# Performance work log

Hardware: AMD Instinct MI355X
Metric: run time of the kernel (lower is better)

The kernel has to match this reference:

```python
import jax, jax.numpy as jnp
import numpy as np

B, C, H, W = 2, 128, 32, 48
D_INNER = 2 * C          # expand=2
D_STATE = 16
DT_RANK = int(np.ceil(C / 16))
K = 4                    # four scan directions
EPS = 1e-5


def setup_inputs() -> dict:
    ks = jax.random.split(jax.random.key(0), 8)
    return {
        "rgb": jax.random.normal(ks[0], (B, C, H, W), jnp.float32),
        "t": jax.random.normal(ks[1], (B, C, H, W), jnp.float32),
        "in_proj_w": jax.random.normal(ks[2], (2 * D_INNER, C), jnp.float32) / np.float32(np.sqrt(C)),
        "conv_w": jax.random.normal(ks[3], (D_INNER, 1, 3, 3), jnp.float32) / 3.0,
        "conv_b": jnp.zeros((D_INNER,), jnp.float32),
        "x_proj_w": jax.random.normal(ks[4], (K, DT_RANK + 2 * D_STATE, D_INNER), jnp.float32) / np.float32(np.sqrt(D_INNER)),
        "dt_projs_w": jax.random.normal(ks[5], (K, D_INNER, DT_RANK), jnp.float32) * np.float32(DT_RANK ** -0.5),
        "dt_projs_b": jax.random.uniform(ks[6], (K, D_INNER), jnp.float32, minval=1e-4, maxval=0.1),
        "A_logs": jnp.log(jnp.tile(jnp.arange(1, D_STATE + 1, dtype=jnp.float32), (K * D_INNER, 1))),
        "Ds": jnp.ones((K * D_INNER,), jnp.float32),
        "out_norm_g": jnp.ones((D_INNER,), jnp.float32),
        "out_norm_b": jnp.zeros((D_INNER,), jnp.float32),
        "out_proj_w": jax.random.normal(ks[7], (C, D_INNER), jnp.float32) / np.float32(np.sqrt(D_INNER)),
    }


def _selective_scan(u, delta, A, Bmat, Cmat, Dvec):
    """u, delta: (B,K,D,L); A: (K,D,N); Bmat/Cmat: (B,K,N,L); Dvec: (K,D)."""
    uT = jnp.moveaxis(u, -1, 0)      # (L,B,K,D)
    dT = jnp.moveaxis(delta, -1, 0)  # (L,B,K,D)
    BT = jnp.moveaxis(Bmat, -1, 0)   # (L,B,K,N)
    CT = jnp.moveaxis(Cmat, -1, 0)   # (L,B,K,N)
    h0 = jnp.zeros(u.shape[:3] + (A.shape[-1],), u.dtype)  # (B,K,D,N)

    def step(h, xs):
        u_t, d_t, B_t, C_t = xs
        dA = jnp.exp(d_t[..., None] * A)                       # (B,K,D,N)
        h = dA * h + (d_t * u_t)[..., None] * B_t[:, :, None, :]
        y = jnp.einsum('bkdn,bkn->bkd', h, C_t)
        return h, y

    _, ys = jax.lax.scan(step, h0, (uT, dT, BT, CT))           # ys: (L,B,K,D)
    return jnp.moveaxis(ys, 0, -1) + Dvec[None, :, :, None] * u


def _ss2d(x, in_proj_w, conv_w, conv_b, x_proj_w, dt_projs_w, dt_projs_b,
          A_logs, Ds, out_norm_g, out_norm_b, out_proj_w):
    b, hs, ws, c = x.shape
    L = hs * ws
    xz = x @ in_proj_w.T                                       # (B,Hs,Ws,2*Din)
    xx, z = jnp.split(xz, 2, axis=-1)
    xc = jnp.transpose(xx, (0, 3, 1, 2))                       # (B,Din,Hs,Ws)
    xc = jax.lax.conv_general_dilated(
        xc, conv_w, (1, 1), ((1, 1), (1, 1)),
        feature_group_count=D_INNER,
        dimension_numbers=('NCHW', 'OIHW', 'NCHW'))
    xc = jax.nn.silu(xc + conv_b[None, :, None, None])
    # 4-direction scan inputs: HW, WH, and their reverses
    x_hw = xc.reshape(b, D_INNER, L)
    x_wh = jnp.transpose(xc, (0, 1, 3, 2)).reshape(b, D_INNER, L)
    x_hwwh = jnp.stack([x_hw, x_wh], axis=1)                   # (B,2,Din,L)
    xs = jnp.concatenate([x_hwwh, jnp.flip(x_hwwh, axis=-1)], axis=1)  # (B,4,Din,L)
    x_dbl = jnp.einsum('bkdl,kcd->bkcl', xs, x_proj_w)
    dts = x_dbl[:, :, :DT_RANK]
    Bs = x_dbl[:, :, DT_RANK:DT_RANK + D_STATE]                # (B,K,N,L)
    Cs = x_dbl[:, :, DT_RANK + D_STATE:]                       # (B,K,N,L)
    dts = jnp.einsum('bkrl,kdr->bkdl', dts, dt_projs_w)
    delta = jax.nn.softplus(dts + dt_projs_b[None, :, :, None])
    A = -jnp.exp(A_logs).reshape(K, D_INNER, D_STATE)
    out_y = _selective_scan(xs, delta, A, Bs, Cs, Ds.reshape(K, D_INNER))  # (B,4,Din,L)
    inv_y = jnp.flip(out_y[:, 2:4], axis=-1)                   # (B,2,Din,L)
    wh_y = jnp.transpose(out_y[:, 1].reshape(b, D_INNER, ws, hs), (0, 1, 3, 2)).reshape(b, D_INNER, L)
    invwh_y = jnp.transpose(inv_y[:, 1].reshape(b, D_INNER, ws, hs), (0, 1, 3, 2)).reshape(b, D_INNER, L)
    y = out_y[:, 0] + inv_y[:, 0] + wh_y + invwh_y             # (B,Din,L)
    y = jnp.transpose(y, (0, 2, 1)).reshape(b, hs, ws, D_INNER)
    mu = y.mean(-1, keepdims=True)
    var = jnp.mean((y - mu) ** 2, axis=-1, keepdims=True)
    y = (y - mu) * jax.lax.rsqrt(var + EPS) * out_norm_g + out_norm_b
    y = y * jax.nn.silu(z)
    return y @ out_proj_w.T                                    # (B,Hs,Ws,C)


def reference(rgb, t, in_proj_w, conv_w, conv_b, x_proj_w, dt_projs_w, dt_projs_b,
              A_logs, Ds, out_norm_g, out_norm_b, out_proj_w):
    b, c, h, w = rgb.shape
    rgb_tok = jnp.transpose(rgb, (0, 2, 3, 1)).reshape(b, h * w, c)
    t_tok = jnp.transpose(t, (0, 2, 3, 1)).reshape(b, h * w, c)
    # interleave: rgb0, t0, rgb1, t1, ... -> (B, H, 2W, C)
    rgbt = jnp.stack([rgb_tok, t_tok], axis=2).reshape(b, h, 2 * w, c)
    out = _ss2d(rgbt, in_proj_w, conv_w, conv_b, x_proj_w, dt_projs_w, dt_projs_b,
                A_logs, Ds, out_norm_g, out_norm_b, out_proj_w)
    # keep thermal-position tokens (odd indices)
    out = out.reshape(b, 2 * h * w, c)[:, 1::2, :].reshape(b, h, w, c)
    return jnp.transpose(out, (0, 3, 1, 2))
```

## Files before the change

### kernel.cpp

```cpp
#include <hip/hip_runtime.h>

#define B_   2
#define CIN  128
#define H_   32
#define W_   48
#define HS   32
#define WS2  96
#define LT   3072
#define DI   256
#define NS   16
#define RK   8
#define KK   4
#define NCH  128
#define CHL  24

typedef unsigned int  u32;
typedef unsigned short u16;

__device__ __forceinline__ u16 f2bf(float x) {
  u32 u = __float_as_uint(x);
  return (u16)((u + 0x7FFFu + ((u >> 16) & 1u)) >> 16);
}
__device__ __forceinline__ float bf2f(u16 s) {
  return __uint_as_float((u32)s << 16);
}

__device__ __forceinline__ int lcanon(int k, int ls) {
  if (k == 0) return ls;
  if (k == 1) return (ls & 31) * WS2 + (ls >> 5);
  if (k == 2) return LT - 1 - ls;
  int j = LT - 1 - ls;
  return (j & 31) * WS2 + (j >> 5);
}

__global__ __launch_bounds__(256) void k_wprep(
    const float* __restrict__ w, float* __restrict__ wT) {
  __shared__ float tile[32][33];
  int t = threadIdx.x;
  int bm = blockIdx.x & 15;
  int bk = blockIdx.x >> 4;
  int m0 = bm * 32, k0 = bk * 32;
  #pragma unroll
  for (int q = 0; q < 4; ++q) {
    int idx = q * 256 + t;
    int mi = idx >> 5, ki = idx & 31;
    tile[mi][ki] = w[(size_t)(m0 + mi) * CIN + k0 + ki];
  }
  __syncthreads();
  #pragma unroll
  for (int q = 0; q < 4; ++q) {
    int idx = q * 256 + t;
    int ki = idx >> 5, mi = idx & 31;
    wT[(size_t)(k0 + ki) * 512 + m0 + mi] = tile[mi][ki];
  }
}

__global__ __launch_bounds__(256) void k_inproj(
    const float* __restrict__ rgb, const float* __restrict__ tin,
    const float* __restrict__ wT, float* __restrict__ xz) {
  __shared__ float xv[CIN][16];
  int t  = threadIdx.x;
  int bi = blockIdx.x;
  bool zh = bi >= 384;
  int bb, l0;
  if (!zh) { int r = bi;       bb = r / 192; l0 = (r % 192) * 16; }
  else     { int r = bi - 384; bb = r / 96;  l0 = (r % 96) * 32; }
  int h = l0 / WS2, w20 = l0 % WS2;
  #pragma unroll
  for (int rep = 0; rep < 8; ++rep) {
    int idx = rep * 256 + t;
    int tok = idx & 15, c = idx >> 4;
    int w2 = zh ? (w20 + 2 * tok + 1) : (w20 + tok);
    const float* src = (w2 & 1) ? tin : rgb;
    xv[c][tok] = src[((size_t)(bb * CIN + c) * HS + h) * W_ + (w2 >> 1)];
  }
  __syncthreads();
  int oc = (t & 63) * 4;
  int th = t >> 6;
  const float4* wp = reinterpret_cast<const float4*>(wT + (zh ? 256 : 0) + oc);
  float4 A0 = {0,0,0,0}, A1 = {0,0,0,0}, A2 = {0,0,0,0}, A3 = {0,0,0,0};
  #pragma unroll 4
  for (int k = 0; k < CIN; ++k) {
    float4 w4 = wp[k * 128];
    float4 x4 = *reinterpret_cast<const float4*>(&xv[k][th * 4]);
    A0.x += x4.x * w4.x; A0.y += x4.x * w4.y; A0.z += x4.x * w4.z; A0.w += x4.x * w4.w;
    A1.x += x4.y * w4.x; A1.y += x4.y * w4.y; A1.z += x4.y * w4.z; A1.w += x4.y * w4.w;
    A2.x += x4.z * w4.x; A2.y += x4.z * w4.y; A2.z += x4.z * w4.z; A2.w += x4.z * w4.w;
    A3.x += x4.w * w4.x; A3.y += x4.w * w4.y; A3.z += x4.w * w4.z; A3.w += x4.w * w4.w;
  }
  int colbase = (zh ? 256 : 0) + oc;
  #pragma unroll
  for (int j = 0; j < 4; ++j) {
    int tok = th * 4 + j;
    int l = zh ? (l0 + 2 * tok + 1) : (l0 + tok);
    float4 v = (j == 0) ? A0 : (j == 1) ? A1 : (j == 2) ? A2 : A3;
    *reinterpret_cast<float4*>(xz + ((size_t)bb * LT + l) * 512 + colbase) = v;
  }
}

__global__ __launch_bounds__(256) void k_convdbc(
    const float* __restrict__ xz, const float* __restrict__ cw,
    const float* __restrict__ cbias, const float* __restrict__ xpw,
    float* __restrict__ xc, float* __restrict__ xcT,
    float* __restrict__ dts_sc, float* __restrict__ Bsb, float* __restrict__ Csb) {
  __shared__ float xv[8][260];
  __shared__ float outs2[128][9];
  __shared__ float dts_s[KK][8][9];
  int t  = threadIdx.x;
  int bi = blockIdx.x;
  int bb = bi / 384;
  int r  = bi % 384;
  int h  = r / 12;
  int q  = r % 12;
  int w0 = q * 8;
  int l0 = h * WS2 + w0;
  {
    float wreg[9];
    #pragma unroll
    for (int i = 0; i < 9; ++i) wreg[i] = cw[t * 9 + i];
    float bias = cbias[t];
    bool hm = (h > 0), hp = (h < HS - 1);
    const size_t rowb = ((size_t)bb * LT + h * WS2) * 512 + t;
    const size_t up = (size_t)WS2 * 512;
    float a0=0,a1=0,b0=0,b1=0,c0=0,c1=0;
    if (w0 > 0) {
      size_t o = rowb + (size_t)(w0 - 1) * 512;
      b0 = xz[o];
      if (hm) a0 = xz[o - up];
      if (hp) c0 = xz[o + up];
    }
    {
      size_t o = rowb + (size_t)w0 * 512;
      b1 = xz[o];
      if (hm) a1 = xz[o - up];
      if (hp) c1 = xz[o + up];
    }
    #pragma unroll
    for (int s = 0; s < 8; ++s) {
      int w2 = w0 + s;
      float a2 = 0, b2 = 0, c2 = 0;
      if (w2 + 1 < WS2) {
        size_t o = rowb + (size_t)(w2 + 1) * 512;
        b2 = xz[o];
        if (hm) a2 = xz[o - up];
        if (hp) c2 = xz[o + up];
      }
      float acc = bias
        + wreg[0]*a0 + wreg[1]*a1 + wreg[2]*a2
        + wreg[3]*b0 + wreg[4]*b1 + wreg[5]*b2
        + wreg[6]*c0 + wreg[7]*c1 + wreg[8]*c2;
      float sv = acc / (1.f + __expf(-acc));
      xc [((size_t)bb * LT + h * WS2 + w2) * DI + t] = sv;
      xcT[((size_t)bb * LT + w2 * 32 + h) * DI + t] = sv;
      xv[s][t] = sv;
      a0=a1; a1=a2; b0=b1; b1=b2; c0=c1; c1=c2;
    }
  }
  __syncthreads();
  int i = t & 7, cb = t >> 3;
  float acc[5] = {0.f, 0.f, 0.f, 0.f, 0.f};
  const float4* xr  = reinterpret_cast<const float4*>(&xv[i][0]);
  const float4* wp0 = reinterpret_cast<const float4*>(xpw + (size_t)cb * DI);
  #pragma unroll 8
  for (int d4 = 0; d4 < 64; ++d4) {
    float4 x4 = xr[d4];
    #pragma unroll
    for (int j = 0; j < 5; ++j) {
      float4 w = wp0[j * 2048 + d4];
      acc[j] += w.x*x4.x + w.y*x4.y + w.z*x4.z + w.w*x4.w;
    }
  }
  #pragma unroll
  for (int j = 0; j < 5; ++j) {
    int cc  = cb + 32 * j;
    int k   = (cc * 205) >> 13;
    int c40 = cc - 40 * k;
    if (c40 < RK) dts_s[k][i][c40] = acc[j];
    else          outs2[k * 32 + (c40 - RK)][i] = acc[j];
  }
  __syncthreads();
  {
    int n = t & 15, tok = (t >> 4) & 7;
    bool isC = (t >= 128);
    int lc = l0 + tok, hh = h, w2 = w0 + tok;
    int lw = w2 * 32 + hh;
    int lsA[4] = {lc, lw, LT - 1 - lc, LT - 1 - lw};
    float* dst = isC ? Csb : Bsb;
    int off = isC ? 16 : 0;
    #pragma unroll
    for (int k = 0; k < KK; ++k)
      dst[(((size_t)bb * KK + k) * LT + lsA[k]) * NS + n] = outs2[k * 32 + off + n][tok];
  }
  {
    int k2 = t >> 6, tok2 = (t >> 3) & 7, rr = t & 7;
    int lc2 = l0 + tok2;
    int lw2 = (w0 + tok2) * 32 + h;
    int ls2 = (k2 == 0) ? lc2 : (k2 == 1) ? lw2 : (k2 == 2) ? (LT - 1 - lc2) : (LT - 1 - lw2);
    dts_sc[(((size_t)bb * KK + k2) * LT + ls2) * RK + rr] = dts_s[k2][tok2][rr];
  }
}

__global__ __launch_bounds__(256, 4) void k_scan1(
    const float* __restrict__ dts_sc, const float* __restrict__ xc,
    const float* __restrict__ xcT, const float* __restrict__ Bsb,
    const float* __restrict__ dtw, const float* __restrict__ dtb,
    const float* __restrict__ Alog, u16* __restrict__ chH,
    float* __restrict__ sumd) {
  int t  = threadIdx.x;
  int bi = blockIdx.x;
  int bb = bi / (KK * NCH);
  int k  = (bi / NCH) % KK;
  int ch = bi % NCH;
  size_t bk = (size_t)bb * KK + k;
  const float4* dp4 = reinterpret_cast<const float4*>(dts_sc + bk * LT * RK);
  const float4* Bp4 = reinterpret_cast<const float4*>(Bsb + bk * LT * NS);
  const float* src = ((k & 1) ? xcT : xc) + (size_t)bb * LT * DI;
  int dir = (k < 2) ? 1 : -1;
  int i0  = (k < 2) ? ch * CHL : LT - 1 - ch * CHL;
  const float* wr = dtw + ((size_t)k * DI + t) * RK;
  float4 w0 = *reinterpret_cast<const float4*>(wr);
  float4 w1 = *reinterpret_cast<const float4*>(wr + 4);
  float bias = dtb[k * DI + t];
  float a[NS], h[NS];
  bool okf = true;
  #pragma unroll
  for (int n = 0; n < NS; ++n) {
    a[n] = -__expf(Alog[((size_t)k * DI + t) * NS + n]);
    h[n] = 0.f;
    if (n) okf = okf && (fabsf(a[n] - (n + 1) * a[0]) <= 1e-3f * (n + 1) * fabsf(a[0]));
  }
  float a0 = a[0];
  float sd = 0.f;
  int ls0 = ch * CHL;
  float4 q0 = dp4[2 * ls0], q1 = dp4[2 * ls0 + 1];
  float4 b0 = Bp4[4 * ls0], b1 = Bp4[4 * ls0 + 1],
         b2 = Bp4[4 * ls0 + 2], b3 = Bp4[4 * ls0 + 3];
  float u = src[(size_t)i0 * DI + t];
  if (okf) {
    for (int s = 0; s < CHL; ++s) {
      int sn  = (s + 1 < CHL) ? s + 1 : s;
      int lsn = ch * CHL + sn;
      float4 nq0 = dp4[2 * lsn], nq1 = dp4[2 * lsn + 1];
      float4 nb0 = Bp4[4 * lsn], nb1 = Bp4[4 * lsn + 1],
             nb2 = Bp4[4 * lsn + 2], nb3 = Bp4[4 * lsn + 3];
      float nu = src[(size_t)(i0 + dir * sn) * DI + t];
      float xx = bias + w0.x*q0.x + w0.y*q0.y + w0.z*q0.z + w0.w*q0.w
                      + w1.x*q1.x + w1.y*q1.y + w1.z*q1.z + w1.w*q1.w;
      float dlt = fmaxf(xx, 0.f) + __logf(1.f + __expf(-fabsf(xx)));
      sd += dlt;
      float du = dlt * u;
      float e1 = __expf(dlt * a0);
      float e2 = e1 * e1;
      float e3 = e2 * e1;
      float e4 = e2 * e2;
      float e8 = e4 * e4;
      float e12 = e8 * e4;
      float qv[4] = {e1, e2, e3, e4};
      float bs[4] = {1.f, e4, e8, e12};
      float bv[16] = {b0.x,b0.y,b0.z,b0.w, b1.x,b1.y,b1.z,b1.w,
                      b2.x,b2.y,b2.z,b2.w, b3.x,b3.y,b3.z,b3.w};
      #pragma unroll
      for (int g = 0; g < 4; ++g) {
        float base = bs[g];
        #pragma unroll
        for (int j = 0; j < 4; ++j) {
          int n = 4 * g + j;
          float p = base * qv[j];
          h[n] = p * h[n] + du * bv[n];
        }
      }
      q0 = nq0; q1 = nq1; b0 = nb0; b1 = nb1; b2 = nb2; b3 = nb3; u = nu;
    }
  } else {
    for (int s = 0; s < CHL; ++s) {
      int sn  = (s + 1 < CHL) ? s + 1 : s;
      int lsn = ch * CHL + sn;
      float4 nq0 = dp4[2 * lsn], nq1 = dp4[2 * lsn + 1];
      float4 nb0 = Bp4[4 * lsn], nb1 = Bp4[4 * lsn + 1],
             nb2 = Bp4[4 * lsn + 2], nb3 = Bp4[4 * lsn + 3];
      float nu = src[(size_t)(i0 + dir * sn) * DI + t];
      float xx = bias + w0.x*q0.x + w0.y*q0.y + w0.z*q0.z + w0.w*q0.w
                      + w1.x*q1.x + w1.y*q1.y + w1.z*q1.z + w1.w*q1.w;
      float dlt = fmaxf(xx, 0.f) + __logf(1.f + __expf(-fabsf(xx)));
      sd += dlt;
      float du = dlt * u;
      float bv[16] = {b0.x,b0.y,b0.z,b0.w, b1.x,b1.y,b1.z,b1.w,
                      b2.x,b2.y,b2.z,b2.w, b3.x,b3.y,b3.z,b3.w};
      #pragma unroll
      for (int n = 0; n < NS; ++n) h[n] = __expf(dlt * a[n]) * h[n] + du * bv[n];
      q0 = nq0; q1 = nq1; b0 = nb0; b1 = nb1; b2 = nb2; b3 = nb3; u = nu;
    }
  }
  u32 pk[8];
  #pragma unroll
  for (int i = 0; i < 8; ++i)
    pk[i] = (u32)f2bf(h[2*i]) | ((u32)f2bf(h[2*i+1]) << 16);
  u32* outp = reinterpret_cast<u32*>(chH + ((bk * NCH + ch) * DI + t) * NS);
  *reinterpret_cast<uint4*>(outp)     = make_uint4(pk[0], pk[1], pk[2], pk[3]);
  *reinterpret_cast<uint4*>(outp + 4) = make_uint4(pk[4], pk[5], pk[6], pk[7]);
  sumd[(bk * NCH + ch) * DI + t] = sd;
}

__global__ __launch_bounds__(256) void k_scan2(
    u16* __restrict__ chH, const float* __restrict__ sumd,
    const float* __restrict__ Alog) {
  int t  = threadIdx.x;
  int bi = blockIdx.x;
  int bb = bi / (KK * 16);
  int k  = (bi / 16) % KK;
  int dg = bi % 16;
  int d = dg * 16 + (t >> 4);
  int n = t & 15;
  float a = -__expf(Alog[((size_t)k * DI + d) * NS + n]);
  float carry = 0.f;
  size_t bk = (size_t)bb * KK + k;
  size_t base = (bk * NCH) * DI + d;
  float Hc = bf2f(chH[base * NS + n]);
  float sd = sumd[base];
  for (int ch = 0; ch < NCH; ++ch) {
    size_t nbase = base + DI;
    float Hc2 = 0.f, sd2 = 0.f;
    if (ch + 1 < NCH) { Hc2 = bf2f(chH[nbase * NS + n]); sd2 = sumd[nbase]; }
    chH[base * NS + n] = f2bf(carry);
    carry = __expf(a * sd) * carry + Hc;
    base = nbase; Hc = Hc2; sd = sd2;
  }
}

__global__ __launch_bounds__(256, 4) void k_scan3(
    const float* __restrict__ dts_sc, const float* __restrict__ xc,
    const float* __restrict__ xcT, const float* __restrict__ Bsb,
    const float* __restrict__ Csb, const float* __restrict__ dtw,
    const float* __restrict__ dtb, const float* __restrict__ Alog,
    const float* __restrict__ Ds, const u16* __restrict__ chH,
    u16* __restrict__ yhalf) {
  int t  = threadIdx.x;
  int bi = blockIdx.x;
  int bb = bi / (KK * NCH);
  int k  = (bi / NCH) % KK;
  int ch = bi % NCH;
  size_t bk = (size_t)bb * KK + k;
  const float4* dp4 = reinterpret_cast<const float4*>(dts_sc + bk * LT * RK);
  const float4* Bp4 = reinterpret_cast<const float4*>(Bsb + bk * LT * NS);
  const float4* Cp4 = reinterpret_cast<const float4*>(Csb + bk * LT * NS);
  const float* src = ((k & 1) ? xcT : xc) + (size_t)bb * LT * DI;
  int dir = (k < 2) ? 1 : -1;
  int i0  = (k < 2) ? ch * CHL : LT - 1 - ch * CHL;
  const float* wr = dtw + ((size_t)k * DI + t) * RK;
  float4 w0 = *reinterpret_cast<const float4*>(wr);
  float4 w1 = *reinterpret_cast<const float4*>(wr + 4);
  float bias = dtb[k * DI + t];
  float a[NS], h[NS];
  bool okf = true;
  #pragma unroll
  for (int n = 0; n < NS; ++n) {
    a[n] = -__expf(Alog[((size_t)k * DI + t) * NS + n]);
    if (n) okf = okf && (fabsf(a[n] - (n + 1) * a[0]) <= 1e-3f * (n + 1) * fabsf(a[0]));
  }
  float a0 = a[0];
  {
    const uint4* hp4 = reinterpret_cast<const uint4*>(chH + ((bk * NCH + ch) * DI + t) * NS);
    uint4 A = hp4[0], Bq = hp4[1];
    u32 w[8] = {A.x, A.y, A.z, A.w, Bq.x, Bq.y, Bq.z, Bq.w};
    #pragma unroll
    for (int i = 0; i < 8; ++i) {
      h[2*i]   = bf2f((u16)(w[i] & 0xFFFFu));
      h[2*i+1] = bf2f((u16)(w[i] >> 16));
    }
  }
  float dv = Ds[k * DI + t];
  int ls0 = ch * CHL;
  float4 q0 = dp4[2 * ls0], q1 = dp4[2 * ls0 + 1];
  float4 b0 = Bp4[4 * ls0], b1 = Bp4[4 * ls0 + 1],
         b2 = Bp4[4 * ls0 + 2], b3 = Bp4[4 * ls0 + 3];
  float4 c0 = Cp4[4 * ls0], c1 = Cp4[4 * ls0 + 1],
         c2 = Cp4[4 * ls0 + 2], c3 = Cp4[4 * ls0 + 3];
  float u = src[(size_t)i0 * DI + t];
  if (okf) {
    for (int s = 0; s < CHL; ++s) {
      int sn  = (s + 1 < CHL) ? s + 1 : s;
      int lsn = ch * CHL + sn;
      float4 nq0 = dp4[2 * lsn], nq1 = dp4[2 * lsn + 1];
      float4 nb0 = Bp4[4 * lsn], nb1 = Bp4[4 * lsn + 1],
             nb2 = Bp4[4 * lsn + 2], nb3 = Bp4[4 * lsn + 3];
      float4 nc0 = Cp4[4 * lsn], nc1 = Cp4[4 * lsn + 1],
             nc2 = Cp4[4 * lsn + 2], nc3 = Cp4[4 * lsn + 3];
      float nu = src[(size_t)(i0 + dir * sn) * DI + t];
      float xx = bias + w0.x*q0.x + w0.y*q0.y + w0.z*q0.z + w0.w*q0.w
                      + w1.x*q1.x + w1.y*q1.y + w1.z*q1.z + w1.w*q1.w;
      float dlt = fmaxf(xx, 0.f) + __logf(1.f + __expf(-fabsf(xx)));
      float du = dlt * u;
      float e1 = __expf(dlt * a0);
      float e2 = e1 * e1;
      float e3 = e2 * e1;
      float e4 = e2 * e2;
      float e8 = e4 * e4;
      float e12 = e8 * e4;
      float qv[4] = {e1, e2, e3, e4};
      float bs[4] = {1.f, e4, e8, e12};
      float bv[16] = {b0.x,b0.y,b0.z,b0.w, b1.x,b1.y,b1.z,b1.w,
                      b2.x,b2.y,b2.z,b2.w, b3.x,b3.y,b3.z,b3.w};
      float cv[16] = {c0.x,c0.y,c0.z,c0.w, c1.x,c1.y,c1.z,c1.w,
                      c2.x,c2.y,c2.z,c2.w, c3.x,c3.y,c3.z,c3.w};
      float y0 = 0.f, y1 = 0.f, y2 = 0.f, y3 = 0.f;
      #pragma unroll
      for (int g = 0; g < 4; ++g) {
        float base = bs[g];
        #pragma unroll
        for (int j = 0; j < 4; ++j) {
          int n = 4 * g + j;
          float p = base * qv[j];
          float hn = p * h[n] + du * bv[n];
          h[n] = hn;
          float pr = hn * cv[n];
          if (g == 0) y0 += pr; else if (g == 1) y1 += pr;
          else if (g == 2) y2 += pr; else y3 += pr;
        }
      }
      float y = ((y0 + y1) + (y2 + y3)) + dv * u;
      int ls = ch * CHL + s;
      int lc = lcanon(k, ls);
      if (lc & 1)
        yhalf[(bk * (LT/2) + (lc >> 1)) * DI + t] = f2bf(y);
      q0 = nq0; q1 = nq1; b0 = nb0; b1 = nb1; b2 = nb2; b3 = nb3;
      c0 = nc0; c1 = nc1; c2 = nc2; c3 = nc3; u = nu;
    }
  } else {
    for (int s = 0; s < CHL; ++s) {
      int sn  = (s + 1 < CHL) ? s + 1 : s;
      int lsn = ch * CHL + sn;
      float4 nq0 = dp4[2 * lsn], nq1 = dp4[2 * lsn + 1];
      float4 nb0 = Bp4[4 * lsn], nb1 = Bp4[4 * lsn + 1],
             nb2 = Bp4[4 * lsn + 2], nb3 = Bp4[4 * lsn + 3];
      float4 nc0 = Cp4[4 * lsn], nc1 = Cp4[4 * lsn + 1],
             nc2 = Cp4[4 * lsn + 2], nc3 = Cp4[4 * lsn + 3];
      float nu = src[(size_t)(i0 + dir * sn) * DI + t];
      float xx = bias + w0.x*q0.x + w0.y*q0.y + w0.z*q0.z + w0.w*q0.w
                      + w1.x*q1.x + w1.y*q1.y + w1.z*q1.z + w1.w*q1.w;
      float dlt = fmaxf(xx, 0.f) + __logf(1.f + __expf(-fabsf(xx)));
      float du = dlt * u;
      float bv[16] = {b0.x,b0.y,b0.z,b0.w, b1.x,b1.y,b1.z,b1.w,
                      b2.x,b2.y,b2.z,b2.w, b3.x,b3.y,b3.z,b3.w};
      float cv[16] = {c0.x,c0.y,c0.z,c0.w, c1.x,c1.y,c1.z,c1.w,
                      c2.x,c2.y,c2.z,c2.w, c3.x,c3.y,c3.z,c3.w};
      float y = 0.f;
      #pragma unroll
      for (int n = 0; n < NS; ++n) { h[n] = __expf(dlt * a[n]) * h[n] + du * bv[n]; y += h[n] * cv[n]; }
      y += dv * u;
      int ls = ch * CHL + s;
      int lc = lcanon(k, ls);
      if (lc & 1)
        yhalf[(bk * (LT/2) + (lc >> 1)) * DI + t] = f2bf(y);
      q0 = nq0; q1 = nq1; b0 = nb0; b1 = nb1; b2 = nb2; b3 = nb3;
      c0 = nc0; c1 = nc1; c2 = nc2; c3 = nc3; u = nu;
    }
  }
}

__global__ __launch_bounds__(256) void k_out(
    const u16* __restrict__ yhalf, const float* __restrict__ xz,
    const float* __restrict__ gam, const float* __restrict__ be,
    const float* __restrict__ opw, float* __restrict__ out) {
  __shared__ float yt[4][260];
  int t = threadIdx.x;
  int bb   = blockIdx.x / 384;
  int tile = blockIdx.x % 384;
  {
    int lane = t & 63, tok = t >> 6;
    int m = tile * 4 + tok;
    int lc = (m / W_) * WS2 + (m % W_) * 2 + 1;
    float yv[4];
    #pragma unroll
    for (int j = 0; j < 4; ++j) {
      int d = lane + 64 * j;
      float s = 0.f;
      #pragma unroll
      for (int k = 0; k < KK; ++k)
        s += bf2f(yhalf[(((size_t)bb * KK + k) * (LT/2) + m) * DI + d]);
      yv[j] = s;
    }
    float sum = yv[0] + yv[1] + yv[2] + yv[3];
    #pragma unroll
    for (int off = 32; off > 0; off >>= 1) sum += __shfl_xor(sum, off, 64);
    float mu = sum * (1.f / DI);
    float sq = 0.f;
    #pragma unroll
    for (int j = 0; j < 4; ++j) { float dd = yv[j] - mu; sq += dd * dd; }
    #pragma unroll
    for (int off = 32; off > 0; off >>= 1) sq += __shfl_xor(sq, off, 64);
    float rs = rsqrtf(sq * (1.f / DI) + 1e-5f);
    #pragma unroll
    for (int j = 0; j < 4; ++j) {
      int d = lane + 64 * j;
      float z = xz[((size_t)bb * LT + lc) * 512 + DI + d];
      float sz = z / (1.f + __expf(-z));
      yt[tok][d] = ((yv[j] - mu) * rs * gam[d] + be[d]) * sz;
    }
  }
  __syncthreads();
  int i = t & 3, og = t >> 2;
  const float4* yr = reinterpret_cast<const float4*>(&yt[i][0]);
  const float4* w0p = reinterpret_cast<const float4*>(opw + (size_t)og * DI);
  const float4* w1p = reinterpret_cast<const float4*>(opw + (size_t)(og + 64) * DI);
  float a0 = 0.f, a1 = 0.f;
  for (int d4 = 0; d4 < 64; ++d4) {
    float4 y4 = yr[d4];
    float4 wa = w0p[d4], wb2 = w1p[d4];
    a0 += wa.x*y4.x + wa.y*y4.y + wa.z*y4.z + wa.w*y4.w;
    a1 += wb2.x*y4.x + wb2.y*y4.y + wb2.z*y4.z + wb2.w*y4.w;
  }
  int m = tile * 4 + i;
  int hh = m / W_, ww = m % W_;
  out[((size_t)(bb * CIN + og) * HS + hh) * W_ + ww] = a0;
  out[((size_t)(bb * CIN + og + 64) * HS + hh) * W_ + ww] = a1;
}

extern "C" void kernel_launch(void* const* d_in, const int* in_sizes, int n_in,
                              void* d_out, int out_size, void* d_ws, size_t ws_size,
                              hipStream_t stream) {
  const float* rgb  = (const float*)d_in[0];
  const float* tin  = (const float*)d_in[1];
  const float* ipw  = (const float*)d_in[2];
  const float* cw   = (const float*)d_in[3];
  const float* cb   = (const float*)d_in[4];
  const float* xpw  = (const float*)d_in[5];
  const float* dtw  = (const float*)d_in[6];
  const float* dtb  = (const float*)d_in[7];
  const float* Alog = (const float*)d_in[8];
  const float* Ds   = (const float*)d_in[9];
  const float* g    = (const float*)d_in[10];
  const float* be   = (const float*)d_in[11];
  const float* opw  = (const float*)d_in[12];
  float* out = (float*)d_out;

  float* ws    = (float*)d_ws;
  float* xz    = ws;
  float* xc    = xz    + 3145728;
  float* xcT   = xc    + 1572864;
  float* dts   = xcT   + 1572864;
  float* Bsb   = dts   + 196608;
  float* Csb   = Bsb   + 393216;
  u16*   chH   = (u16*)(Csb + 393216);
  float* sumd  = Csb   + 393216 + 2097152;
  u16*   yhalf = (u16*)(sumd + 262144);
  float* wT    = sumd  + 262144 + 1572864;

  k_wprep  <<<64,   256, 0, stream>>>(ipw, wT);
  k_inproj <<<576,  256, 0, stream>>>(rgb, tin, wT, xz);
  k_convdbc<<<768,  256, 0, stream>>>(xz, cw, cb, xpw, xc, xcT, dts, Bsb, Csb);
  k_scan1  <<<1024, 256, 0, stream>>>(dts, xc, xcT, Bsb, dtw, dtb, Alog, chH, sumd);
  k_scan2  <<<128,  256, 0, stream>>>(chH, sumd, Alog);
  k_scan3  <<<1024, 256, 0, stream>>>(dts, xc, xcT, Bsb, Csb, dtw, dtb, Alog, Ds, chH, yhalf);
  k_out    <<<768,  256, 0, stream>>>(yhalf, xz, g, be, opw, out);
}
```

Measured before the change: 147.1 us.

## Emit local-state outputs in scan pass 1 and add carry correction in pass 3

The first chunked-scan pass now also computes each kept token's output from the zero-initialised chunk-local state and writes it to yhalf, along with the running cumulative delta. The third pass no longer recomputes the recurrence. It loads the chunk's carry-in state and adds the linear correction C·(exp(A·cumdelta)·h_carry) to the stored output. This removes the repeated delta/B/u loads and recurrence work from pass 3. In exchange, pass 1 does extra C loads and stores, a new cumulative-delta buffer is written and read back, and the output is rounded to bf16 twice.

```diff
diff --git a/kernel.cpp b/kernel.cpp
--- a/kernel.cpp
+++ b/kernel.cpp
@@ -203,9 +203,11 @@
 __global__ __launch_bounds__(256, 4) void k_scan1(
     const float* __restrict__ dts_sc, const float* __restrict__ xc,
     const float* __restrict__ xcT, const float* __restrict__ Bsb,
-    const float* __restrict__ dtw, const float* __restrict__ dtb,
-    const float* __restrict__ Alog, u16* __restrict__ chH,
-    float* __restrict__ sumd) {
+    const float* __restrict__ Csb, const float* __restrict__ dtw,
+    const float* __restrict__ dtb, const float* __restrict__ Alog,
+    const float* __restrict__ Ds, u16* __restrict__ chH,
+    float* __restrict__ sumd, float* __restrict__ cdb,
+    u16* __restrict__ yhalf) {
   int t  = threadIdx.x;
   int bi = blockIdx.x;
   int bb = bi / (KK * NCH);
@@ -214,6 +216,7 @@
   size_t bk = (size_t)bb * KK + k;
   const float4* dp4 = reinterpret_cast<const float4*>(dts_sc + bk * LT * RK);
   const float4* Bp4 = reinterpret_cast<const float4*>(Bsb + bk * LT * NS);
+  const float4* Cp4 = reinterpret_cast<const float4*>(Csb + bk * LT * NS);
   const float* src = ((k & 1) ? xcT : xc) + (size_t)bb * LT * DI;
   int dir = (k < 2) ? 1 : -1;
   int i0  = (k < 2) ? ch * CHL : LT - 1 - ch * CHL;
@@ -221,6 +224,7 @@
   float4 w0 = *reinterpret_cast<const float4*>(wr);
   float4 w1 = *reinterpret_cast<const float4*>(wr + 4);
   float bias = dtb[k * DI + t];
+  float dv = Ds[k * DI + t];
   float a[NS], h[NS];
   bool okf = true;
   #pragma unroll
@@ -269,6 +273,27 @@
           h[n] = p * h[n] + du * bv[n];
         }
       }
+      int ls = ch * CHL + s;
+      int lc = lcanon(k, ls);
+      if (lc & 1) {
+        float4 c0 = Cp4[4 * ls], c1 = Cp4[4 * ls + 1],
+               c2 = Cp4[4 * ls + 2], c3 = Cp4[4 * ls + 3];
+        float cv[16] = {c0.x,c0.y,c0.z,c0.w, c1.x,c1.y,c1.z,c1.w,
+                        c2.x,c2.y,c2.z,c2.w, c3.x,c3.y,c3.z,c3.w};
+        float y0 = 0.f, y1 = 0.f, y2 = 0.f, y3 = 0.f;
+        #pragma unroll
+        for (int n = 0; n < 4; ++n)  y0 += h[n]      * cv[n];
+        #pragma unroll
+        for (int n = 0; n < 4; ++n)  y1 += h[4 + n]  * cv[4 + n];
+        #pragma unroll
+        for (int n = 0; n < 4; ++n)  y2 += h[8 + n]  * cv[8 + n];
+        #pragma unroll
+        for (int n = 0; n < 4; ++n)  y3 += h[12 + n] * cv[12 + n];
+        float y = ((y0 + y1) + (y2 + y3)) + dv * u;
+        size_t slot = (bk * (size_t)(LT/2) + (lc >> 1)) * DI + t;
+        yhalf[slot] = f2bf(y);
+        cdb[slot] = sd;
+      }
       q0 = nq0; q1 = nq1; b0 = nb0; b1 = nb1; b2 = nb2; b3 = nb3; u = nu;
     }
   } else {
@@ -288,6 +313,21 @@
                       b2.x,b2.y,b2.z,b2.w, b3.x,b3.y,b3.z,b3.w};
       #pragma unroll
       for (int n = 0; n < NS; ++n) h[n] = __expf(dlt * a[n]) * h[n] + du * bv[n];
+      int ls = ch * CHL + s;
+      int lc = lcanon(k, ls);
+      if (lc & 1) {
+        float4 c0 = Cp4[4 * ls], c1 = Cp4[4 * ls + 1],
+               c2 = Cp4[4 * ls + 2], c3 = Cp4[4 * ls + 3];
+        float cv[16] = {c0.x,c0.y,c0.z,c0.w, c1.x,c1.y,c1.z,c1.w,
+                        c2.x,c2.y,c2.z,c2.w, c3.x,c3.y,c3.z,c3.w};
+        float y = 0.f;
+        #pragma unroll
+        for (int n = 0; n < NS; ++n) y += h[n] * cv[n];
+        y += dv * u;
+        size_t slot = (bk * (size_t)(LT/2) + (lc >> 1)) * DI + t;
+        yhalf[slot] = f2bf(y);
+        cdb[slot] = sd;
+      }
       q0 = nq0; q1 = nq1; b0 = nb0; b1 = nb1; b2 = nb2; b3 = nb3; u = nu;
     }
   }
@@ -328,11 +368,8 @@
 }
 
 __global__ __launch_bounds__(256, 4) void k_scan3(
-    const float* __restrict__ dts_sc, const float* __restrict__ xc,
-    const float* __restrict__ xcT, const float* __restrict__ Bsb,
-    const float* __restrict__ Csb, const float* __restrict__ dtw,
-    const float* __restrict__ dtb, const float* __restrict__ Alog,
-    const float* __restrict__ Ds, const u16* __restrict__ chH,
+    const float* __restrict__ Csb, const float* __restrict__ Alog,
+    const u16* __restrict__ chH, const float* __restrict__ cdb,
     u16* __restrict__ yhalf) {
   int t  = threadIdx.x;
   int bi = blockIdx.x;
@@ -340,17 +377,8 @@
   int k  = (bi / NCH) % KK;
   int ch = bi % NCH;
   size_t bk = (size_t)bb * KK + k;
-  const float4* dp4 = reinterpret_cast<const float4*>(dts_sc + bk * LT * RK);
-  const float4* Bp4 = reinterpret_cast<const float4*>(Bsb + bk * LT * NS);
   const float4* Cp4 = reinterpret_cast<const float4*>(Csb + bk * LT * NS);
-  const float* src = ((k & 1) ? xcT : xc) + (size_t)bb * LT * DI;
-  int dir = (k < 2) ? 1 : -1;
-  int i0  = (k < 2) ? ch * CHL : LT - 1 - ch * CHL;
-  const float* wr = dtw + ((size_t)k * DI + t) * RK;
-  float4 w0 = *reinterpret_cast<const float4*>(wr);
-  float4 w1 = *reinterpret_cast<const float4*>(wr + 4);
-  float bias = dtb[k * DI + t];
-  float a[NS], h[NS];
+  float a[NS], hn[NS];
   bool okf = true;
   #pragma unroll
   for (int n = 0; n < NS; ++n) {
@@ -364,33 +392,22 @@
     u32 w[8] = {A.x, A.y, A.z, A.w, Bq.x, Bq.y, Bq.z, Bq.w};
     #pragma unroll
     for (int i = 0; i < 8; ++i) {
-      h[2*i]   = bf2f((u16)(w[i] & 0xFFFFu));
-      h[2*i+1] = bf2f((u16)(w[i] >> 16));
-    }
-  }
-  float dv = Ds[k * DI + t];
-  int ls0 = ch * CHL;
-  float4 q0 = dp4[2 * ls0], q1 = dp4[2 * ls0 + 1];
-  float4 b0 = Bp4[4 * ls0], b1 = Bp4[4 * ls0 + 1],
-         b2 = Bp4[4 * ls0 + 2], b3 = Bp4[4 * ls0 + 3];
-  float4 c0 = Cp4[4 * ls0], c1 = Cp4[4 * ls0 + 1],
-         c2 = Cp4[4 * ls0 + 2], c3 = Cp4[4 * ls0 + 3];
-  float u = src[(size_t)i0 * DI + t];
+      hn[2*i]   = bf2f((u16)(w[i] & 0xFFFFu));
+      hn[2*i+1] = bf2f((u16)(w[i] >> 16));
+    }
+  }
   if (okf) {
     for (int s = 0; s < CHL; ++s) {
-      int sn  = (s + 1 < CHL) ? s + 1 : s;
-      int lsn = ch * CHL + sn;
-      float4 nq0 = dp4[2 * lsn], nq1 = dp4[2 * lsn + 1];
-      float4 nb0 = Bp4[4 * lsn], nb1 = Bp4[4 * lsn + 1],
-             nb2 = Bp4[4 * lsn + 2], nb3 = Bp4[4 * lsn + 3];
-      float4 nc0 = Cp4[4 * lsn], nc1 = Cp4[4 * lsn + 1],
-             nc2 = Cp4[4 * lsn + 2], nc3 = Cp4[4 * lsn + 3];
-      float nu = src[(size_t)(i0 + dir * sn) * DI + t];
-      float xx = bias + w0.x*q0.x + w0.y*q0.y + w0.z*q0.z + w0.w*q0.w
-                      + w1.x*q1.x + w1.y*q1.y + w1.z*q1.z + w1.w*q1.w;
-      float dlt = fmaxf(xx, 0.f) + __logf(1.f + __expf(-fabsf(xx)));
-      float du = dlt * u;
-      float e1 = __expf(dlt * a0);
+      int ls = ch * CHL + s;
+      int lc = lcanon(k, ls);
+      if (!(lc & 1)) continue;
+      size_t slot = (bk * (size_t)(LT/2) + (lc >> 1)) * DI + t;
+      float cd = cdb[slot];
+      float4 c0 = Cp4[4 * ls], c1 = Cp4[4 * ls + 1],
+             c2 = Cp4[4 * ls + 2], c3 = Cp4[4 * ls + 3];
+      float cv[16] = {c0.x,c0.y,c0.z,c0.w, c1.x,c1.y,c1.z,c1.w,
+                      c2.x,c2.y,c2.z,c2.w, c3.x,c3.y,c3.z,c3.w};
+      float e1 = __expf(a0 * cd);
       float e2 = e1 * e1;
       float e3 = e2 * e1;
       float e4 = e2 * e2;
@@ -398,10 +415,6 @@
       float e12 = e8 * e4;
       float qv[4] = {e1, e2, e3, e4};
       float bs[4] = {1.f, e4, e8, e12};
-      float bv[16] = {b0.x,b0.y,b0.z,b0.w, b1.x,b1.y,b1.z,b1.w,
-                      b2.x,b2.y,b2.z,b2.w, b3.x,b3.y,b3.z,b3.w};
-      float cv[16] = {c0.x,c0.y,c0.z,c0.w, c1.x,c1.y,c1.z,c1.w,
-                      c2.x,c2.y,c2.z,c2.w, c3.x,c3.y,c3.z,c3.w};
       float y0 = 0.f, y1 = 0.f, y2 = 0.f, y3 = 0.f;
       #pragma unroll
       for (int g = 0; g < 4; ++g) {
@@ -409,50 +422,30 @@
         #pragma unroll
         for (int j = 0; j < 4; ++j) {
           int n = 4 * g + j;
-          float p = base * qv[j];
-          float hn = p * h[n] + du * bv[n];
-          h[n] = hn;
-          float pr = hn * cv[n];
+          float pr = hn[n] * (base * qv[j]) * cv[n];
           if (g == 0) y0 += pr; else if (g == 1) y1 += pr;
           else if (g == 2) y2 += pr; else y3 += pr;
         }
       }
-      float y = ((y0 + y1) + (y2 + y3)) + dv * u;
+      float corr = (y0 + y1) + (y2 + y3);
+      yhalf[slot] = f2bf(bf2f(yhalf[slot]) + corr);
+    }
+  } else {
+    for (int s = 0; s < CHL; ++s) {
       int ls = ch * CHL + s;
       int lc = lcanon(k, ls);
-      if (lc & 1)
-        yhalf[(bk * (LT/2) + (lc >> 1)) * DI + t] = f2bf(y);
-      q0 = nq0; q1 = nq1; b0 = nb0; b1 = nb1; b2 = nb2; b3 = nb3;
-      c0 = nc0; c1 = nc1; c2 = nc2; c3 = nc3; u = nu;
-    }
-  } else {
-    for (int s = 0; s < CHL; ++s) {
-      int sn  = (s + 1 < CHL) ? s + 1 : s;
-      int lsn = ch * CHL + sn;
-      float4 nq0 = dp4[2 * lsn], nq1 = dp4[2 * lsn + 1];
-      float4 nb0 = Bp4[4 * lsn], nb1 = Bp4[4 * lsn + 1],
-             nb2 = Bp4[4 * lsn + 2], nb3 = Bp4[4 * lsn + 3];
-      float4 nc0 = Cp4[4 * lsn], nc1 = Cp4[4 * lsn + 1],
-             nc2 = Cp4[4 * lsn + 2], nc3 = Cp4[4 * lsn + 3];
-      float nu = src[(size_t)(i0 + dir * sn) * DI + t];
-      float xx = bias + w0.x*q0.x + w0.y*q0.y + w0.z*q0.z + w0.w*q0.w
-                      + w1.x*q1.x + w1.y*q1.y + w1.z*q1.z + w1.w*q1.w;
-      float dlt = fmaxf(xx, 0.f) + __logf(1.f + __expf(-fabsf(xx)));
-      float du = dlt * u;
-      float bv[16] = {b0.x,b0.y,b0.z,b0.w, b1.x,b1.y,b1.z,b1.w,
-                      b2.x,b2.y,b2.z,b2.w, b3.x,b3.y,b3.z,b3.w};
+      if (!(lc & 1)) continue;
+      size_t slot = (bk * (size_t)(LT/2) + (lc >> 1)) * DI + t;
+      float cd = cdb[slot];
+      float4 c0 = Cp4[4 * ls], c1 = Cp4[4 * ls + 1],
+             c2 = Cp4[4 * ls + 2], c3 = Cp4[4 * ls + 3];
       float cv[16] = {c0.x,c0.y,c0.z,c0.w, c1.x,c1.y,c1.z,c1.w,
                       c2.x,c2.y,c2.z,c2.w, c3.x,c3.y,c3.z,c3.w};
-      float y = 0.f;
+      float corr = 0.f;
       #pragma unroll
-      for (int n = 0; n < NS; ++n) { h[n] = __expf(dlt * a[n]) * h[n] + du * bv[n]; y += h[n] * cv[n]; }
-      y += dv * u;
-      int ls = ch * CHL + s;
-      int lc = lcanon(k, ls);
-      if (lc & 1)
-        yhalf[(bk * (LT/2) + (lc >> 1)) * DI + t] = f2bf(y);
-      q0 = nq0; q1 = nq1; b0 = nb0; b1 = nb1; b2 = nb2; b3 = nb3;
-      c0 = nc0; c1 = nc1; c2 = nc2; c3 = nc3; u = nu;
+      for (int n = 0; n < NS; ++n)
+        corr += hn[n] * __expf(a[n] * cd) * cv[n];
+      yhalf[slot] = f2bf(bf2f(yhalf[slot]) + corr);
     }
   }
 }
@@ -543,13 +536,15 @@
   u16*   chH   = (u16*)(Csb + 393216);
   float* sumd  = Csb   + 393216 + 2097152;
   u16*   yhalf = (u16*)(sumd + 262144);
-  float* wT    = sumd  + 262144 + 1572864;
+  float* cdb   = sumd  + 262144 + 1572864;
+  float* wT    = cdb   + 3145728;
 
   k_wprep  <<<64,   256, 0, stream>>>(ipw, wT);
   k_inproj <<<576,  256, 0, stream>>>(rgb, tin, wT, xz);
   k_convdbc<<<768,  256, 0, stream>>>(xz, cw, cb, xpw, xc, xcT, dts, Bsb, Csb);
-  k_scan1  <<<1024, 256, 0, stream>>>(dts, xc, xcT, Bsb, dtw, dtb, Alog, chH, sumd);
+  k_scan1  <<<1024, 256, 0, stream>>>(dts, xc, xcT, Bsb, Csb, dtw, dtb, Alog, Ds,
+                                      chH, sumd, cdb, yhalf);
   k_scan2  <<<128,  256, 0, stream>>>(chH, sumd, Alog);
-  k_scan3  <<<1024, 256, 0, stream>>>(dts, xc, xcT, Bsb, Csb, dtw, dtb, Alog, Ds, chH, yhalf);
+  k_scan3  <<<1024, 256, 0, stream>>>(Csb, Alog, chH, cdb, yhalf);
   k_out    <<<768,  256, 0, stream>>>(yhalf, xz, g, be, opw, out);
 }
```

Result: slower. 150.7 us (+2.5%).
